# Kernel tuning notes

Hardware: AMD Instinct MI355X
Metric: run time of the kernel (lower is better)

The kernel has to match this reference:

```python
import jax, jax.numpy as jnp
import numpy as np

B, T, C, H = 4, 2048, 1024, 16
D = C // H  # head_dim = 64


def setup_inputs() -> dict:
    key = jax.random.key(0)
    k1, k2, k3, k4, k5 = jax.random.split(key, 5)
    x = jax.random.normal(k1, (B, T, C), dtype=jnp.float32)
    # torch nn.Linear weights: [out_features, in_features]
    s = 1.0 / np.sqrt(C)
    qkv_w = jax.random.uniform(k2, (3 * C, C), dtype=jnp.float32, minval=-s, maxval=s)
    qkv_b = jax.random.uniform(k3, (3 * C,), dtype=jnp.float32, minval=-s, maxval=s)
    out_w = jax.random.uniform(k4, (C, C), dtype=jnp.float32, minval=-s, maxval=s)
    out_b = jax.random.uniform(k5, (C,), dtype=jnp.float32, minval=-s, maxval=s)
    # causal mask broadcastable to [B,H,T,T]; 0 (False) marks masked positions
    attn_mask = jnp.tril(jnp.ones((T, T), dtype=bool))[None, None]
    return {"x": x, "qkv_w": qkv_w, "qkv_b": qkv_b, "out_w": out_w,
            "out_b": out_b, "attn_mask": attn_mask}


def reference(x, qkv_w, qkv_b, out_w, out_b, attn_mask):
    qkv = x @ qkv_w.T + qkv_b                      # [B,T,3C]
    q, k, v = jnp.split(qkv, 3, axis=-1)
    # [B,T,C] -> [B,H,T,D]
    q = q.reshape(B, T, H, D).transpose(0, 2, 1, 3)
    k = k.reshape(B, T, H, D).transpose(0, 2, 1, 3)
    v = v.reshape(B, T, H, D).transpose(0, 2, 1, 3)
    scale = 1.0 / np.sqrt(D)
    attn = jnp.einsum('bhqd,bhkd->bhqk', q, k) * scale   # [B,H,T,T]
    neg = jnp.finfo(attn.dtype).min
    attn = jnp.where(attn_mask, attn, neg)
    attn = jax.nn.softmax(attn, axis=-1)
    out = jnp.einsum('bhqk,bhkd->bhqd', attn, v)          # [B,H,T,D]
    out = out.transpose(0, 2, 1, 3).reshape(B, T, C)
    return out @ out_w.T + out_b
```

## Files before the change

kernel.cpp:

```cpp
#include <hip/hip_runtime.h>
#include <hip/hip_bf16.h>

#define B_ 4
#define T_ 2048
#define C_ 1024
#define H_ 16
#define D_ 64

typedef __hip_bfloat16 bf16;
typedef float f32x4 __attribute__((ext_vector_type(4)));
typedef short bf16s8 __attribute__((ext_vector_type(8)));

#define NEG_BIG (-1e30f)

__device__ inline unsigned short f2bf(float f) {
  __hip_bfloat16 h = __float2bfloat16(f);
  return *reinterpret_cast<unsigned short*>(&h);
}
__device__ inline float bf_lo(unsigned u) {
  union { unsigned u; float f; } c; c.u = u << 16; return c.f;
}

__device__ inline void async_load16(const void* g, void* l) {
  __builtin_amdgcn_global_load_lds(
      (const __attribute__((address_space(1))) unsigned int*)g,
      (__attribute__((address_space(3))) unsigned int*)l, 16, 0, 0);
}

__device__ inline void plswap32(unsigned& a, unsigned& b) {
  auto r = __builtin_amdgcn_permlane32_swap(a, b, false, false);
  a = r[0]; b = r[1];
}
__device__ inline void plswap16(unsigned& a, unsigned& b) {
  auto r = __builtin_amdgcn_permlane16_swap(a, b, false, false);
  a = r[0]; b = r[1];
}

union U4 { uint4 u; unsigned short s[8]; };

__device__ inline uint4 load8(const void* base, size_t idx, int f32) {
  if (f32) {
    const float* p = (const float*)base + idx;
    float4 a = *(const float4*)p;
    float4 b = *(const float4*)(p + 4);
    U4 r;
    r.s[0] = f2bf(a.x); r.s[1] = f2bf(a.y); r.s[2] = f2bf(a.z); r.s[3] = f2bf(a.w);
    r.s[4] = f2bf(b.x); r.s[5] = f2bf(b.y); r.s[6] = f2bf(b.z); r.s[7] = f2bf(b.w);
    return r.u;
  }
  return *(const uint4*)((const unsigned short*)base + idx);
}

__global__ void detect_k(const unsigned short* __restrict__ w, int* __restrict__ flag) {
  int lane = threadIdx.x;
  bool big = false;
  for (int i = lane; i < 512; i += 64) {
    float f = bf_lo((unsigned)w[i]);
    if (!(fabsf(f) <= 1.0f)) big = true;
  }
  int any = __any(big);
  if (lane == 0) *flag = any ? 1 : 0;
}

#define R_X   1048576
#define R_WQ  (R_X + 393216)
#define R_WO  (R_WQ + 131072)
#define R_BQ  (R_WO + 384)
#define R_BO  (R_BQ + 128)
__global__ __launch_bounds__(256) void convert_all_k(
    const void* __restrict__ x, const void* __restrict__ wq,
    const void* __restrict__ wo, const void* __restrict__ bq,
    const void* __restrict__ bo,
    bf16* __restrict__ xd, bf16* __restrict__ wqd, bf16* __restrict__ wod,
    bf16* __restrict__ bqd, bf16* __restrict__ bod,
    const int* __restrict__ flag) {
  const int f32 = *flag;
  long long g = (long long)blockIdx.x * 256 + threadIdx.x;
  if (g >= R_BO) return;
  const void* src; bf16* dst; long long base;
  if (g < R_X)       { src = x;  dst = xd;  base = 0; }
  else if (g < R_WQ) { src = wq; dst = wqd; base = R_X; }
  else if (g < R_WO) { src = wo; dst = wod; base = R_WQ; }
  else if (g < R_BQ) { src = bq; dst = bqd; base = R_WO; }
  else               { src = bo; dst = bod; base = R_BQ; }
  size_t i = (size_t)(g - base) * 8;
  *(uint4*)(dst + i) = load8(src, i, f32);
}

template <int KDIM, int MROWS>
__device__ inline void gemm_core(const bf16* __restrict__ A,
                                 const bf16* __restrict__ W,
                                 int tm, int tn, int wm, int wn,
                                 f32x4 acc[MROWS / 32][4], bf16* As, bf16* Bs) {
  const int tid  = threadIdx.x;
  const int lane = tid & 63;
  const int rl   = lane & 15;
  const int kq   = (lane >> 4) * 8;

  for (int k0 = 0; k0 < KDIM; k0 += 32) {
    __syncthreads();
#pragma unroll
    for (int j = 0; j < MROWS / 64; ++j) {
      int f    = j * 4096 + tid * 16;
      int row  = f >> 6;
      int colb = f & 63;
      async_load16((const char*)A + ((size_t)(tm + row) * KDIM + k0) * 2 + colb,
                   (char*)As + f);
    }
#pragma unroll
    for (int j = 0; j < 2; ++j) {
      int f    = j * 4096 + tid * 16;
      int row  = f >> 6;
      int colb = f & 63;
      async_load16((const char*)W + ((size_t)(tn + row) * KDIM + k0) * 2 + colb,
                   (char*)Bs + f);
    }
    __syncthreads();

    bf16s8 af[MROWS / 32], bw[4];
#pragma unroll
    for (int mt = 0; mt < MROWS / 32; ++mt)
      af[mt] = *(const bf16s8*)(As + (wm + mt * 16 + rl) * 32 + kq);
#pragma unroll
    for (int nt = 0; nt < 4; ++nt)
      bw[nt] = *(const bf16s8*)(Bs + (wn + nt * 16 + rl) * 32 + kq);

#pragma unroll
    for (int mt = 0; mt < MROWS / 32; ++mt)
#pragma unroll
      for (int nt = 0; nt < 4; ++nt)
        acc[mt][nt] = __builtin_amdgcn_mfma_f32_16x16x32_bf16(af[mt], bw[nt],
                                                              acc[mt][nt], 0, 0, 0);
  }
}

#define CSTRIDE 72
#define FSTRIDE 68

__global__ __launch_bounds__(256) void gemm_qkv_k(
    const bf16* __restrict__ X, const bf16* __restrict__ W,
    const bf16* __restrict__ bias,
    bf16* __restrict__ q, bf16* __restrict__ k, bf16* __restrict__ v) {
  __shared__ __align__(16) char smem[4 * 64 * CSTRIDE * 2];
  bf16* As = (bf16*)smem;
  bf16* Bs = (bf16*)(smem + 8192);
  const int tid = threadIdx.x;
  const int wave = tid >> 6, lane = tid & 63;
  const int tm = blockIdx.x * 128, tn = blockIdx.y * 128;
  const int wm = (wave >> 1) * 64, wn = (wave & 1) * 64;
  f32x4 acc[4][4];
#pragma unroll
  for (int i = 0; i < 4; ++i)
#pragma unroll
    for (int j = 0; j < 4; ++j) acc[i][j] = 0.0f;

  gemm_core<C_, 128>(X, W, tm, tn, wm, wn, acc, As, Bs);

  __syncthreads();
  bf16* Cs = (bf16*)smem + wave * 64 * CSTRIDE;

  const int rl = lane & 15, qd = lane >> 4;
  const int nbase = tn + wn;
  const int which = nbase >> 10;
  const int h = (nbase & 1023) >> 6;
  const float sc = which == 0 ? 0.125f : 1.0f;
  const int mbase = tm + wm;
  const int b = mbase >> 11, t0 = mbase & 2047;
  bf16* dst = which == 0 ? q : (which == 1 ? k : v);
  bf16* base = dst + (((size_t)(b * H_ + h)) * T_ + t0) * D_;

#pragma unroll
  for (int nt = 0; nt < 4; ++nt) {
    float bv = __bfloat162float(bias[nbase + nt * 16 + rl]);
#pragma unroll
    for (int mt = 0; mt < 4; ++mt)
#pragma unroll
      for (int r = 0; r < 4; ++r)
        Cs[(mt * 16 + qd * 4 + r) * CSTRIDE + nt * 16 + rl] =
            __float2bfloat16((acc[mt][nt][r] + bv) * sc);
  }
#pragma unroll
  for (int it = 0; it < 8; ++it) {
    int row = it * 8 + (lane >> 3);
    uint4 val = *(const uint4*)(Cs + row * CSTRIDE + (lane & 7) * 8);
    *(uint4*)(base + row * D_ + (lane & 7) * 8) = val;
  }
}

__global__ __launch_bounds__(256) void gemm_out_k(
    const bf16* __restrict__ O, const bf16* __restrict__ W,
    const bf16* __restrict__ bias, const int* __restrict__ flag,
    void* __restrict__ out) {
  __shared__ __align__(16) char smem[4 * 32 * FSTRIDE * 4];
  bf16* As = (bf16*)smem;
  bf16* Bs = (bf16*)(smem + 4096);
  const int f32 = *flag;
  const int tid = threadIdx.x;
  const int wave = tid >> 6, lane = tid & 63;
  const int tm = blockIdx.x * 64, tn = blockIdx.y * 128;
  const int wm = (wave >> 1) * 32, wn = (wave & 1) * 64;
  f32x4 acc[2][4];
#pragma unroll
  for (int i = 0; i < 2; ++i)
#pragma unroll
    for (int j = 0; j < 4; ++j) acc[i][j] = 0.0f;

  gemm_core<C_, 64>(O, W, tm, tn, wm, wn, acc, As, Bs);

  __syncthreads();
  const int rl = lane & 15, qd = lane >> 4;

  if (f32) {
    float* Cs = (float*)(smem + wave * 32 * FSTRIDE * 4);
#pragma unroll
    for (int nt = 0; nt < 4; ++nt) {
      float bv = __bfloat162float(bias[tn + wn + nt * 16 + rl]);
#pragma unroll
      for (int mt = 0; mt < 2; ++mt)
#pragma unroll
        for (int r = 0; r < 4; ++r)
          Cs[(mt * 16 + qd * 4 + r) * FSTRIDE + nt * 16 + rl] = acc[mt][nt][r] + bv;
    }
    float* obase = (float*)out + (size_t)(tm + wm) * C_ + tn + wn;
#pragma unroll
    for (int it = 0; it < 8; ++it) {
      int row = it * 4 + (lane >> 4);
      float4 val = *(const float4*)(Cs + row * FSTRIDE + (lane & 15) * 4);
      *(float4*)(obase + (size_t)row * C_ + (lane & 15) * 4) = val;
    }
  } else {
    bf16* Cs = (bf16*)(smem + wave * 32 * FSTRIDE * 4);
#pragma unroll
    for (int nt = 0; nt < 4; ++nt) {
      float bv = __bfloat162float(bias[tn + wn + nt * 16 + rl]);
#pragma unroll
      for (int mt = 0; mt < 2; ++mt)
#pragma unroll
        for (int r = 0; r < 4; ++r)
          Cs[(mt * 16 + qd * 4 + r) * CSTRIDE + nt * 16 + rl] =
              __float2bfloat16(acc[mt][nt][r] + bv);
    }
    bf16* obase = (bf16*)out + (size_t)(tm + wm) * C_ + tn + wn;
#pragma unroll
    for (int it = 0; it < 4; ++it) {
      int row = it * 8 + (lane >> 3);
      uint4 val = *(const uint4*)(Cs + row * CSTRIDE + (lane & 7) * 8);
      *(uint4*)(obase + (size_t)row * C_ + (lane & 7) * 8) = val;
    }
  }
}

__global__ __launch_bounds__(256) void fattn_k(
    const bf16* __restrict__ q, const bf16* __restrict__ k,
    const bf16* __restrict__ v, bf16* __restrict__ o) {
  __shared__ __align__(16) bf16 Ks[2][64 * 64];
  __shared__ __align__(16) bf16 Vs[2][64 * 64];
  const int tid = threadIdx.x, wave = tid >> 6, lane = tid & 63;
  const int rl = lane & 15, quad = lane >> 4;
  const int bh = blockIdx.x;
  const int b = bh >> 4, h = bh & 15;
  const size_t bhT = (size_t)bh * T_;
  const int sw0 = (quad ^ (rl & 7)) << 3;
  const int sw1 = ((quad | 4) ^ (rl & 7)) << 3;

  bf16s8 ones;
#pragma unroll
  for (int i = 0; i < 8; ++i) ones[i] = (short)0x3F80;

  const int qb = 31 - blockIdx.y;
  const int q0 = qb * 64;

  const int kr0 = tid >> 3;
  const int kc0 = ((tid & 7) ^ (kr0 & 7)) << 4;
  const char* kstage = (const char*)k + (bhT + kr0) * (D_ * 2) + kc0;

  const int kp = tid & 31, dg = tid >> 5;
  const bf16* vstage = v + (bhT + 2 * kp) * D_ + dg * 8;

  const bf16* qr = q + (bhT + q0 + wave * 16 + rl) * D_;
  bf16s8 qf0 = *(const bf16s8*)(qr + quad * 8);
  bf16s8 qf1 = *(const bf16s8*)(qr + 32 + quad * 8);

  f32x4 oacc[4], lacc;
#pragma unroll
  for (int nt = 0; nt < 4; ++nt) oacc[nt] = 0.0f;
  lacc = 0.0f;

  const int nchunk = qb + 1;

  {
    async_load16(kstage, (char*)Ks[0] + tid * 16);
    async_load16(kstage + 32 * 128, (char*)Ks[0] + 4096 + tid * 16);
    uint4 va = *(const uint4*)(vstage);
    uint4 vb = *(const uint4*)(vstage + D_);
    const unsigned* au = (const unsigned*)&va;
    const unsigned* bu = (const unsigned*)&vb;
#pragma unroll
    for (int m = 0; m < 4; ++m) {
      unsigned lo = (au[m] & 0xffffu) | (bu[m] << 16);
      unsigned hi = (au[m] >> 16) | (bu[m] & 0xffff0000u);
      int d0 = dg * 8 + 2 * m;
      int o0 = d0 * 64 + (((kp >> 2) ^ (2 * m)) << 3) + 2 * (kp & 3);
      int o1 = (d0 + 1) * 64 + (((kp >> 2) ^ (2 * m + 1)) << 3) + 2 * (kp & 3);
      *(unsigned*)(Vs[0] + o0) = lo;
      *(unsigned*)(Vs[0] + o1) = hi;
    }
  }
  __syncthreads();

  int cur = 0;
#pragma unroll 1
  for (int c = 0; c < nchunk; ++c) {
    const bf16* Kc = Ks[cur];
    const bf16* Vc = Vs[cur];
    const bool pf = (c + 1 < nchunk);

    uint4 va, vb;
    if (pf) {
      const char* ks = kstage + (size_t)(c + 1) * 8192;
      char* kd = (char*)Ks[cur ^ 1] + tid * 16;
      async_load16(ks, kd);
      async_load16(ks + 32 * 128, kd + 4096);
      const bf16* vs = vstage + (size_t)(c + 1) * 4096;
      va = *(const uint4*)(vs);
      vb = *(const uint4*)(vs + D_);
    }

    const int t0 = q0 + wave * 16;
    const int k0 = c << 6;

    f32x4 s[4];
#pragma unroll
    for (int nt = 0; nt < 4; ++nt) s[nt] = 0.0f;
    __builtin_amdgcn_s_setprio(1);
#pragma unroll
    for (int nt = 0; nt < 4; ++nt) {
      int key = nt * 16 + rl;
      bf16s8 kb0 = *(const bf16s8*)(Kc + key * 64 + sw0);
      bf16s8 kb1 = *(const bf16s8*)(Kc + key * 64 + sw1);
      s[nt] = __builtin_amdgcn_mfma_f32_16x16x32_bf16(kb0, qf0, s[nt], 0, 0, 0);
      s[nt] = __builtin_amdgcn_mfma_f32_16x16x32_bf16(kb1, qf1, s[nt], 0, 0, 0);
    }
    __builtin_amdgcn_s_setprio(0);

    if (c == nchunk - 1) {
      int t = t0 + rl;
#pragma unroll
      for (int nt = 0; nt < 4; ++nt)
#pragma unroll
        for (int r = 0; r < 4; ++r) {
          int key = k0 + nt * 16 + quad * 4 + r;
          if (key > t) s[nt][r] = NEG_BIG;
        }
    }

    unsigned pk[4][2];
#pragma unroll
    for (int nt = 0; nt < 4; ++nt) {
#pragma unroll
      for (int r = 0; r < 4; ++r)
        s[nt][r] = __expf(fminf(s[nt][r], 30.0f));
      pk[nt][0] = (unsigned)f2bf(s[nt][0]) | ((unsigned)f2bf(s[nt][1]) << 16);
      pk[nt][1] = (unsigned)f2bf(s[nt][2]) | ((unsigned)f2bf(s[nt][3]) << 16);
    }

    union { unsigned w[4]; bf16s8 v; } u0, u1;
    {
      unsigned a = pk[0][0], bq_ = pk[1][0];
      plswap32(a, bq_); plswap16(a, bq_);
      u0.w[0] = a; u0.w[2] = bq_;
      a = pk[0][1]; bq_ = pk[1][1];
      plswap32(a, bq_); plswap16(a, bq_);
      u0.w[1] = a; u0.w[3] = bq_;
      a = pk[2][0]; bq_ = pk[3][0];
      plswap32(a, bq_); plswap16(a, bq_);
      u1.w[0] = a; u1.w[2] = bq_;
      a = pk[2][1]; bq_ = pk[3][1];
      plswap32(a, bq_); plswap16(a, bq_);
      u1.w[1] = a; u1.w[3] = bq_;
    }
    bf16s8 pa0 = u0.v, pa1 = u1.v;

    __builtin_amdgcn_s_setprio(1);
    lacc = __builtin_amdgcn_mfma_f32_16x16x32_bf16(pa0, ones, lacc, 0, 0, 0);
    lacc = __builtin_amdgcn_mfma_f32_16x16x32_bf16(pa1, ones, lacc, 0, 0, 0);
#pragma unroll
    for (int nt = 0; nt < 4; ++nt) {
      int d = nt * 16 + rl;
      bf16s8 vb0 = *(const bf16s8*)(Vc + d * 64 + sw0);
      bf16s8 vb1 = *(const bf16s8*)(Vc + d * 64 + sw1);
      oacc[nt] = __builtin_amdgcn_mfma_f32_16x16x32_bf16(pa0, vb0, oacc[nt], 0, 0, 0);
      oacc[nt] = __builtin_amdgcn_mfma_f32_16x16x32_bf16(pa1, vb1, oacc[nt], 0, 0, 0);
    }
    __builtin_amdgcn_s_setprio(0);

    if (pf) {
      bf16* Vn = Vs[cur ^ 1];
      const unsigned* au = (const unsigned*)&va;
      const unsigned* bu = (const unsigned*)&vb;
#pragma unroll
      for (int m = 0; m < 4; ++m) {
        unsigned lo = (au[m] & 0xffffu) | (bu[m] << 16);
        unsigned hi = (au[m] >> 16) | (bu[m] & 0xffff0000u);
        int d0 = dg * 8 + 2 * m;
        int o0 = d0 * 64 + (((kp >> 2) ^ (2 * m)) << 3) + 2 * (kp & 3);
        int o1 = (d0 + 1) * 64 + (((kp >> 2) ^ (2 * m + 1)) << 3) + 2 * (kp & 3);
        *(unsigned*)(Vn + o0) = lo;
        *(unsigned*)(Vn + o1) = hi;
      }
    }
    __syncthreads();
    cur ^= 1;
  }

  f32x4 linv;
#pragma unroll
  for (int r = 0; r < 4; ++r) linv[r] = 1.0f / lacc[r];
#pragma unroll
  for (int nt = 0; nt < 4; ++nt) {
    int d = nt * 16 + rl;
#pragma unroll
    for (int r = 0; r < 4; ++r) {
      int t = q0 + wave * 16 + quad * 4 + r;
      o[((size_t)b * T_ + t) * C_ + h * D_ + d] =
          __float2bfloat16(oacc[nt][r] * linv[r]);
    }
  }
}

extern "C" void kernel_launch(void* const* d_in, const int* in_sizes, int n_in,
                              void* d_out, int out_size, void* d_ws, size_t ws_size,
                              hipStream_t stream) {
  (void)in_sizes; (void)n_in; (void)out_size; (void)ws_size;
  const void* x     = d_in[0];
  const void* qkv_w = d_in[1];
  const void* qkv_b = d_in[2];
  const void* out_w = d_in[3];
  const void* out_b = d_in[4];

  const size_t nqkv = (size_t)B_ * T_ * C_;
  char* ws = (char*)d_ws;
  int*  flag = (int*)ws;
  bf16* q   = (bf16*)(ws + 256);
  bf16* kk  = q + nqkv;
  bf16* vv  = kk + nqkv;
  bf16* oo  = vv + nqkv;
  bf16* xbf = oo;
  bf16* wqkv = oo + nqkv;
  bf16* wout = wqkv + 3 * C_ * C_;
  bf16* bqkv = wout + C_ * C_;
  bf16* bout = bqkv + 3 * C_;

  detect_k<<<1, 64, 0, stream>>>((const unsigned short*)qkv_w, flag);
  convert_all_k<<<(R_BO + 255) / 256, 256, 0, stream>>>(
      x, qkv_w, out_w, qkv_b, out_b, xbf, wqkv, wout, bqkv, bout, flag);

  gemm_qkv_k<<<dim3(64, 24), 256, 0, stream>>>(xbf, wqkv, bqkv, q, kk, vv);
  fattn_k<<<dim3(64, 32), 256, 0, stream>>>(q, kk, vv, oo);
  gemm_out_k<<<dim3(128, 8), 256, 0, stream>>>(oo, wout, bout, flag, d_out);
}
```

Before: 270.1 us.

## Store V transposed from QKV GEMM and async-load it in attention

The QKV projection epilogue now writes V in a [B,H,D,T] transposed layout via an LDS transpose. The attention kernel can then stage V tiles with the same async global-to-LDS loads and swizzle used for K. This replaces the per-chunk register loads, bit-shuffle repacking and LDS stores. It removes VALU work and register pressure from the attention inner loop and overlaps V loads asynchronously. The cost is a more scattered LDS write pattern in the GEMM epilogue for V tiles.

```diff
diff --git a/kernel.cpp b/kernel.cpp
--- a/kernel.cpp
+++ b/kernel.cpp
@@ -163,27 +163,47 @@
   const int nbase = tn + wn;
   const int which = nbase >> 10;
   const int h = (nbase & 1023) >> 6;
-  const float sc = which == 0 ? 0.125f : 1.0f;
   const int mbase = tm + wm;
   const int b = mbase >> 11, t0 = mbase & 2047;
-  bf16* dst = which == 0 ? q : (which == 1 ? k : v);
-  bf16* base = dst + (((size_t)(b * H_ + h)) * T_ + t0) * D_;
-
-#pragma unroll
-  for (int nt = 0; nt < 4; ++nt) {
-    float bv = __bfloat162float(bias[nbase + nt * 16 + rl]);
-#pragma unroll
-    for (int mt = 0; mt < 4; ++mt)
-#pragma unroll
-      for (int r = 0; r < 4; ++r)
-        Cs[(mt * 16 + qd * 4 + r) * CSTRIDE + nt * 16 + rl] =
-            __float2bfloat16((acc[mt][nt][r] + bv) * sc);
-  }
-#pragma unroll
-  for (int it = 0; it < 8; ++it) {
-    int row = it * 8 + (lane >> 3);
-    uint4 val = *(const uint4*)(Cs + row * CSTRIDE + (lane & 7) * 8);
-    *(uint4*)(base + row * D_ + (lane & 7) * 8) = val;
+
+  if (which == 2) {
+#pragma unroll
+    for (int nt = 0; nt < 4; ++nt) {
+      float bv = __bfloat162float(bias[nbase + nt * 16 + rl]);
+#pragma unroll
+      for (int mt = 0; mt < 4; ++mt)
+#pragma unroll
+        for (int r = 0; r < 4; ++r)
+          Cs[(nt * 16 + rl) * CSTRIDE + mt * 16 + qd * 4 + r] =
+              __float2bfloat16(acc[mt][nt][r] + bv);
+    }
+    bf16* vbase = v + ((size_t)(b * H_ + h) * D_) * T_ + t0;
+#pragma unroll
+    for (int it = 0; it < 8; ++it) {
+      int row = it * 8 + (lane >> 3);
+      uint4 val = *(const uint4*)(Cs + row * CSTRIDE + (lane & 7) * 8);
+      *(uint4*)(vbase + (size_t)row * T_ + (lane & 7) * 8) = val;
+    }
+  } else {
+    const float sc = which == 0 ? 0.125f : 1.0f;
+    bf16* dst = which == 0 ? q : k;
+    bf16* base = dst + (((size_t)(b * H_ + h)) * T_ + t0) * D_;
+#pragma unroll
+    for (int nt = 0; nt < 4; ++nt) {
+      float bv = __bfloat162float(bias[nbase + nt * 16 + rl]);
+#pragma unroll
+      for (int mt = 0; mt < 4; ++mt)
+#pragma unroll
+        for (int r = 0; r < 4; ++r)
+          Cs[(mt * 16 + qd * 4 + r) * CSTRIDE + nt * 16 + rl] =
+              __float2bfloat16((acc[mt][nt][r] + bv) * sc);
+    }
+#pragma unroll
+    for (int it = 0; it < 8; ++it) {
+      int row = it * 8 + (lane >> 3);
+      uint4 val = *(const uint4*)(Cs + row * CSTRIDE + (lane & 7) * 8);
+      *(uint4*)(base + row * D_ + (lane & 7) * 8) = val;
+    }
   }
 }
 
@@ -252,7 +272,7 @@
 
 __global__ __launch_bounds__(256) void fattn_k(
     const bf16* __restrict__ q, const bf16* __restrict__ k,
-    const bf16* __restrict__ v, bf16* __restrict__ o) {
+    const bf16* __restrict__ vT, bf16* __restrict__ o) {
   __shared__ __align__(16) bf16 Ks[2][64 * 64];
   __shared__ __align__(16) bf16 Vs[2][64 * 64];
   const int tid = threadIdx.x, wave = tid >> 6, lane = tid & 63;
@@ -273,9 +293,7 @@
   const int kr0 = tid >> 3;
   const int kc0 = ((tid & 7) ^ (kr0 & 7)) << 4;
   const char* kstage = (const char*)k + (bhT + kr0) * (D_ * 2) + kc0;
-
-  const int kp = tid & 31, dg = tid >> 5;
-  const bf16* vstage = v + (bhT + 2 * kp) * D_ + dg * 8;
+  const char* vstage = (const char*)vT + ((size_t)bh * D_ + kr0) * (T_ * 2) + kc0;
 
   const bf16* qr = q + (bhT + q0 + wave * 16 + rl) * D_;
   bf16s8 qf0 = *(const bf16s8*)(qr + quad * 8);
@@ -289,22 +307,12 @@
   const int nchunk = qb + 1;
 
   {
-    async_load16(kstage, (char*)Ks[0] + tid * 16);
-    async_load16(kstage + 32 * 128, (char*)Ks[0] + 4096 + tid * 16);
-    uint4 va = *(const uint4*)(vstage);
-    uint4 vb = *(const uint4*)(vstage + D_);
-    const unsigned* au = (const unsigned*)&va;
-    const unsigned* bu = (const unsigned*)&vb;
-#pragma unroll
-    for (int m = 0; m < 4; ++m) {
-      unsigned lo = (au[m] & 0xffffu) | (bu[m] << 16);
-      unsigned hi = (au[m] >> 16) | (bu[m] & 0xffff0000u);
-      int d0 = dg * 8 + 2 * m;
-      int o0 = d0 * 64 + (((kp >> 2) ^ (2 * m)) << 3) + 2 * (kp & 3);
-      int o1 = (d0 + 1) * 64 + (((kp >> 2) ^ (2 * m + 1)) << 3) + 2 * (kp & 3);
-      *(unsigned*)(Vs[0] + o0) = lo;
-      *(unsigned*)(Vs[0] + o1) = hi;
-    }
+    char* kd = (char*)Ks[0] + tid * 16;
+    async_load16(kstage, kd);
+    async_load16(kstage + 4096, kd + 4096);
+    char* vd = (char*)Vs[0] + tid * 16;
+    async_load16(vstage, vd);
+    async_load16(vstage + 131072, vd + 4096);
   }
   __syncthreads();
 
@@ -315,15 +323,15 @@
     const bf16* Vc = Vs[cur];
     const bool pf = (c + 1 < nchunk);
 
-    uint4 va, vb;
     if (pf) {
-      const char* ks = kstage + (size_t)(c + 1) * 8192;
+      const size_t ak = (size_t)(c + 1) * 8192;
       char* kd = (char*)Ks[cur ^ 1] + tid * 16;
-      async_load16(ks, kd);
-      async_load16(ks + 32 * 128, kd + 4096);
-      const bf16* vs = vstage + (size_t)(c + 1) * 4096;
-      va = *(const uint4*)(vs);
-      vb = *(const uint4*)(vs + D_);
+      async_load16(kstage + ak, kd);
+      async_load16(kstage + ak + 4096, kd + 4096);
+      const size_t av = (size_t)(c + 1) * 128;
+      char* vd = (char*)Vs[cur ^ 1] + tid * 16;
+      async_load16(vstage + av, vd);
+      async_load16(vstage + av + 131072, vd + 4096);
     }
 
     const int t0 = q0 + wave * 16;
@@ -394,21 +402,6 @@
     }
     __builtin_amdgcn_s_setprio(0);
 
-    if (pf) {
-      bf16* Vn = Vs[cur ^ 1];
-      const unsigned* au = (const unsigned*)&va;
-      const unsigned* bu = (const unsigned*)&vb;
-#pragma unroll
-      for (int m = 0; m < 4; ++m) {
-        unsigned lo = (au[m] & 0xffffu) | (bu[m] << 16);
-        unsigned hi = (au[m] >> 16) | (bu[m] & 0xffff0000u);
-        int d0 = dg * 8 + 2 * m;
-        int o0 = d0 * 64 + (((kp >> 2) ^ (2 * m)) << 3) + 2 * (kp & 3);
-        int o1 = (d0 + 1) * 64 + (((kp >> 2) ^ (2 * m + 1)) << 3) + 2 * (kp & 3);
-        *(unsigned*)(Vn + o0) = lo;
-        *(unsigned*)(Vn + o1) = hi;
-      }
-    }
     __syncthreads();
     cur ^= 1;
   }
```

After: 264.7 us. 2.0% less time.
